# Kernel tuning notes

Measured on AMD Instinct MI355X. Metric: run time of the kernel, lower is better.

The kernel has to match this reference:

```python
import jax, jax.numpy as jnp
import numpy as np

B, S, E, H = 2, 2048, 2048, 16
NOPE, ROPE, VD = 128, 64, 128
QH = NOPE + ROPE  # 192
LORA = 512
ROPE_THETA = 10000.0
EPS = 1e-6


def setup_inputs() -> dict:
    key = jax.random.key(0)
    ks = jax.random.split(key, 5)
    sd = lambda n: 1.0 / np.sqrt(n)
    return {
        "x": jax.random.normal(ks[0], (B, S, E), jnp.float32),
        "wq": jax.random.normal(ks[1], (E, H * QH), jnp.float32) * sd(E),
        "wkv_a": jax.random.normal(ks[2], (E, LORA + ROPE), jnp.float32) * sd(E),
        "wkv_b": jax.random.normal(ks[3], (LORA, H * (NOPE + VD)), jnp.float32) * sd(LORA),
        "wo": jax.random.normal(ks[4], (H * VD, E), jnp.float32) * sd(H * VD),
        "kv_norm_scale": jnp.ones((LORA,), jnp.float32),
    }


def _rope(xp, cos, sin):
    # xp: (..., s, d); cos/sin: (s, d//2)
    d2 = xp.shape[-1] // 2
    x1, x2 = xp[..., :d2], xp[..., d2:]
    return jnp.concatenate([x1 * cos - x2 * sin, x2 * cos + x1 * sin], axis=-1)


def reference(x, wq, wkv_a, wkv_b, wo, kv_norm_scale):
    b, s, _ = x.shape
    # queries: (b, H, s, QH), split into no-pe / pe slices
    q = (x @ wq).reshape(b, s, H, QH).transpose(0, 2, 1, 3)
    q_nope, q_pe = q[..., :NOPE], q[..., NOPE:]

    # low-rank KV latent projection
    kva = x @ wkv_a  # (b, s, LORA + ROPE)
    ckv, k_pe = kva[..., :LORA], kva[..., LORA:]
    ckv = ckv * jax.lax.rsqrt(jnp.mean(ckv * ckv, axis=-1, keepdims=True) + EPS)
    ckv = ckv * kv_norm_scale  # RMSNorm on latent
    kv = (ckv @ wkv_b).reshape(b, s, H, NOPE + VD).transpose(0, 2, 1, 3)
    k_nope, v = kv[..., :NOPE], kv[..., NOPE:]

    # partial RoPE on the rope slice only
    pos = jnp.arange(s, dtype=jnp.float32)
    inv = 1.0 / (ROPE_THETA ** (jnp.arange(0, ROPE, 2, dtype=jnp.float32) / ROPE))
    ang = pos[:, None] * inv  # (s, ROPE//2)
    cos, sin = jnp.cos(ang), jnp.sin(ang)
    q_pe = _rope(q_pe, cos, sin)                 # (b, H, s, ROPE)
    k_pe = _rope(k_pe[:, None, :, :], cos, sin)  # (b, 1, s, ROPE), shared over heads

    # concat (the new_empty + slice-write in torch)
    qs = jnp.concatenate([q_nope, q_pe], axis=-1)  # (b, H, s, QH)
    ks_ = jnp.concatenate(
        [k_nope, jnp.broadcast_to(k_pe, (b, H, s, ROPE))], axis=-1
    )  # (b, H, s, QH)

    # causal SDPA with scale = q_head_dim**-0.5; asymmetric V head dim
    scale = QH ** -0.5
    scores = jnp.einsum('bhqd,bhkd->bhqk', qs, ks_) * scale
    causal = jnp.tril(jnp.ones((s, s), dtype=bool))
    scores = jnp.where(causal, scores, jnp.finfo(scores.dtype).min)
    attn = jax.nn.softmax(scores, axis=-1)
    out = jnp.einsum('bhqk,bhkd->bhqd', attn, v)  # (b, H, s, VD)
    out = out.transpose(0, 2, 1, 3).reshape(b, s, H * VD)
    return out @ wo
```

## Files before the change

### kernel.cpp

```cpp
#include <hip/hip_runtime.h>
#include <stdint.h>
#include <stddef.h>

typedef __bf16 bf16x8 __attribute__((ext_vector_type(8)));
typedef float floatx4 __attribute__((ext_vector_type(4)));
typedef unsigned short u16;

__device__ __forceinline__ float bf2f(u16 h) {
    unsigned u = ((unsigned)h) << 16;
    return __builtin_bit_cast(float, u);
}
__device__ __forceinline__ u16 f2bf(float f) {
    unsigned u = __builtin_bit_cast(unsigned, f);
    u += 0x7fffu + ((u >> 16) & 1u);
    return (u16)(u >> 16);
}

__device__ __forceinline__ void gload16(const void* g, void* l) {
    __builtin_amdgcn_global_load_lds(
        (const __attribute__((address_space(1))) uint32_t*)g,
        (__attribute__((address_space(3))) uint32_t*)l, 16, 0, 0);
}

__device__ __forceinline__ void wait_vm8() { asm volatile("s_waitcnt vmcnt(8)" ::: "memory"); }
__device__ __forceinline__ void wait_vm6() { asm volatile("s_waitcnt vmcnt(6)" ::: "memory"); }
__device__ __forceinline__ void wait_vm4() { asm volatile("s_waitcnt vmcnt(4)" ::: "memory"); }
__device__ __forceinline__ void wait_vm3() { asm volatile("s_waitcnt vmcnt(3)" ::: "memory"); }
__device__ __forceinline__ void wait_vm0() { asm volatile("s_waitcnt vmcnt(0)" ::: "memory"); }

__global__ __launch_bounds__(256) void k_conv_x(const float* __restrict__ in,
                                                u16* __restrict__ out, int n8) {
    int i = blockIdx.x * 256 + threadIdx.x;
    if (i >= n8) return;
    const float* f = in + (size_t)i * 8;
    unsigned o[4];
    for (int t = 0; t < 4; t++) {
        u16 lo = f2bf(f[2 * t]), hi = f2bf(f[2 * t + 1]);
        o[t] = (unsigned)lo | ((unsigned)hi << 16);
    }
    uint4 p = {o[0], o[1], o[2], o[3]};
    *(uint4*)&out[(size_t)i * 8] = p;
}

__global__ __launch_bounds__(256) void k_convT(const float* __restrict__ in,
                                               u16* __restrict__ out, int K, int N) {
    __shared__ u16 t[32][33];
    int k0 = blockIdx.x * 32, n0 = blockIdx.y * 32;
    int c = threadIdx.x & 31, r8 = threadIdx.x >> 5;
    for (int j = 0; j < 4; j++) {
        int row = r8 + j * 8;
        int n = n0 + c;
        t[row][c] = (n < N) ? f2bf(in[(size_t)(k0 + row) * N + n]) : (u16)0;
    }
    __syncthreads();
    for (int j = 0; j < 4; j++) {
        int row = r8 + j * 8;
        out[(size_t)(n0 + row) * K + k0 + c] = t[c][row];
    }
}

template <int NWC, int MODE>
__global__ __launch_bounds__(512, 2) void k_gemm256(const u16* __restrict__ A,
                                                    const u16* __restrict__ BT,
                                                    void* __restrict__ C0,
                                                    void* __restrict__ C1,
                                                    int K, int ldc) {
    constexpr int MFR = 16 / (8 / NWC);
    constexpr int ACH = 2;
    constexpr int BCH = NWC / 2;
    constexpr int SLOT = 8192 + NWC * 2048;
    __shared__ __align__(16) u16 RING[4][SLOT];
    int tid = threadIdx.x;
    int w = tid >> 6, lane = tid & 63;
    int l15 = lane & 15, quad = lane >> 4;
    int wr = w / NWC, wc = w % NWC;

    int gx = gridDim.x;
    int nwg = gx * gridDim.y;
    int flat = blockIdx.y * gx + blockIdx.x;
    int cpx = nwg >> 3;
    int swz = (flat & 7) * cpx + (flat >> 3);
    int bx = swz % gx, by = swz / gx;
    size_t m0 = (size_t)bx * 256, n0 = (size_t)by * (NWC * 64);
    int NT = K >> 5;

    const u16* srcA[ACH];
    const u16* srcB[BCH];
    int ldsAb[ACH], ldsBb[BCH];
#pragma unroll
    for (int p = 0; p < ACH; p++) {
        int chunk = p * 512 + tid;
        int s = chunk >> 6;
        int b = (chunk & 63) * 8;
        int bu = b ^ (((b >> 8) & 1) << 4);
        int r = bu >> 5, c = bu & 31;
        srcA[p] = A + (m0 + s * 16 + r) * (size_t)K + c;
        ldsAb[p] = (p * 512 + w * 64) * 8;
    }
#pragma unroll
    for (int p = 0; p < BCH; p++) {
        int chunk = p * 512 + tid;
        int s = chunk >> 6;
        int b = (chunk & 63) * 8;
        int bu = b ^ (((b >> 8) & 1) << 4);
        int r = bu >> 5, c = bu & 31;
        srcB[p] = BT + (n0 + s * 16 + r) * (size_t)K + c;
        ldsBb[p] = 8192 + (p * 512 + w * 64) * 8;
    }

    const int swb = (l15 * 32 + quad * 8) ^ ((l15 >> 3) << 4);

    floatx4 acc[MFR][4];
    const floatx4 fzero = {0.f, 0.f, 0.f, 0.f};
#pragma unroll
    for (int i = 0; i < MFR; i++)
#pragma unroll
        for (int j = 0; j < 4; j++) acc[i][j] = fzero;

    bf16x8 aA0[MFR], bB0[4], aA1[MFR], bB1[4];

    auto STAGE = [&](int j) {
        int rs = j & 3;
        size_t ko = (size_t)j * 32;
        u16* ring = &RING[rs][0];
#pragma unroll
        for (int p = 0; p < ACH; p++) gload16(srcA[p] + ko, ring + ldsAb[p]);
#pragma unroll
        for (int p = 0; p < BCH; p++) gload16(srcB[p] + ko, ring + ldsBb[p]);
    };
    auto READ0 = [&](int rs) {
        const u16* ring = &RING[rs][0];
#pragma unroll
        for (int i2 = 0; i2 < MFR; i2++)
            aA0[i2] = *(const bf16x8*)&ring[(wr * MFR + i2) * 512 + swb];
#pragma unroll
        for (int j2 = 0; j2 < 4; j2++)
            bB0[j2] = *(const bf16x8*)&ring[8192 + (wc * 4 + j2) * 512 + swb];
    };
    auto READ1 = [&](int rs) {
        const u16* ring = &RING[rs][0];
#pragma unroll
        for (int i2 = 0; i2 < MFR; i2++)
            aA1[i2] = *(const bf16x8*)&ring[(wr * MFR + i2) * 512 + swb];
#pragma unroll
        for (int j2 = 0; j2 < 4; j2++)
            bB1[j2] = *(const bf16x8*)&ring[8192 + (wc * 4 + j2) * 512 + swb];
    };
    auto MMA0 = [&]() {
#pragma unroll
        for (int i2 = 0; i2 < MFR; i2++)
#pragma unroll
            for (int j2 = 0; j2 < 4; j2++)
                acc[i2][j2] = __builtin_amdgcn_mfma_f32_16x16x32_bf16(
                    aA0[i2], bB0[j2], acc[i2][j2], 0, 0, 0);
    };
    auto MMA1 = [&]() {
#pragma unroll
        for (int i2 = 0; i2 < MFR; i2++)
#pragma unroll
            for (int j2 = 0; j2 < 4; j2++)
                acc[i2][j2] = __builtin_amdgcn_mfma_f32_16x16x32_bf16(
                    aA1[i2], bB1[j2], acc[i2][j2], 0, 0, 0);
    };

    STAGE(0); STAGE(1); STAGE(2);

    if constexpr (NWC == 4) {
        auto QSTEP = [&](int rs, bool doStage, int sj) {
            const u16* ring = &RING[rs][0];
#pragma unroll
            for (int i2 = 0; i2 < 4; i2++)
                aA0[i2] = *(const bf16x8*)&ring[(wr * 8 + i2) * 512 + swb];
#pragma unroll
            for (int j2 = 0; j2 < 2; j2++)
                bB0[j2] = *(const bf16x8*)&ring[8192 + (wc * 4 + j2) * 512 + swb];
            __builtin_amdgcn_sched_barrier(0);
#pragma unroll
            for (int j2 = 2; j2 < 4; j2++)
                bB0[j2] = *(const bf16x8*)&ring[8192 + (wc * 4 + j2) * 512 + swb];
            __builtin_amdgcn_sched_barrier(0);
#pragma unroll
            for (int i2 = 0; i2 < 4; i2++)
#pragma unroll
                for (int j2 = 0; j2 < 2; j2++)
                    acc[i2][j2] = __builtin_amdgcn_mfma_f32_16x16x32_bf16(
                        aA0[i2], bB0[j2], acc[i2][j2], 0, 0, 0);
            __builtin_amdgcn_sched_barrier(0);
#pragma unroll
            for (int i2 = 4; i2 < 8; i2++)
                aA0[i2] = *(const bf16x8*)&ring[(wr * 8 + i2) * 512 + swb];
            __builtin_amdgcn_sched_barrier(0);
#pragma unroll
            for (int i2 = 0; i2 < 4; i2++)
#pragma unroll
                for (int j2 = 2; j2 < 4; j2++)
                    acc[i2][j2] = __builtin_amdgcn_mfma_f32_16x16x32_bf16(
                        aA0[i2], bB0[j2], acc[i2][j2], 0, 0, 0);
            __builtin_amdgcn_sched_barrier(0);
            if (doStage) STAGE(sj);
            __builtin_amdgcn_sched_barrier(0);
#pragma unroll
            for (int i2 = 4; i2 < 8; i2++)
#pragma unroll
                for (int j2 = 2; j2 < 4; j2++)
                    acc[i2][j2] = __builtin_amdgcn_mfma_f32_16x16x32_bf16(
                        aA0[i2], bB0[j2], acc[i2][j2], 0, 0, 0);
#pragma unroll
            for (int i2 = 4; i2 < 8; i2++)
#pragma unroll
                for (int j2 = 0; j2 < 2; j2++)
                    acc[i2][j2] = __builtin_amdgcn_mfma_f32_16x16x32_bf16(
                        aA0[i2], bB0[j2], acc[i2][j2], 0, 0, 0);
        };
        int j = 0;
        for (; j + 3 < NT; j++) {
            wait_vm8();
            __builtin_amdgcn_s_barrier();
            __builtin_amdgcn_sched_barrier(0);
            QSTEP(j & 3, true, j + 3);
        }
        {
            wait_vm8();
            __builtin_amdgcn_s_barrier();
            __builtin_amdgcn_sched_barrier(0);
            QSTEP(j & 3, false, 0); j++;
        }
        {
            wait_vm4();
            __builtin_amdgcn_s_barrier();
            __builtin_amdgcn_sched_barrier(0);
            QSTEP(j & 3, false, 0); j++;
        }
        {
            wait_vm0();
            __builtin_amdgcn_s_barrier();
            __builtin_amdgcn_sched_barrier(0);
            QSTEP(j & 3, false, 0);
        }
    } else {
        wait_vm6();
        __builtin_amdgcn_s_barrier();
        __builtin_amdgcn_sched_barrier(0);
        READ0(0);
        for (int j = 0; j + 1 < NT; j += 2) {
            if (j + 2 < NT) wait_vm3(); else wait_vm0();
            __builtin_amdgcn_s_barrier();
            __builtin_amdgcn_sched_barrier(0);
            READ1((j + 1) & 3);
            if (j + 3 < NT) STAGE(j + 3);
            MMA0();
            if (j + 2 < NT) {
                if (j + 3 < NT) wait_vm3(); else wait_vm0();
                __builtin_amdgcn_s_barrier();
                __builtin_amdgcn_sched_barrier(0);
                READ0((j + 2) & 3);
                if (j + 4 < NT) STAGE(j + 4);
            }
            MMA1();
        }
    }

#pragma unroll
    for (int i = 0; i < MFR; i++)
#pragma unroll
        for (int j2 = 0; j2 < 4; j2++) {
            size_t col = n0 + wc * 64 + j2 * 16 + l15;
#pragma unroll
            for (int r = 0; r < 4; r++) {
                size_t row = m0 + (size_t)wr * (MFR * 16) + i * 16 + quad * 4 + r;
                if constexpr (MODE == 0) {
                    ((u16*)C0)[row * ldc + col] = f2bf(acc[i][j2][r]);
                } else if constexpr (MODE == 1) {
                    ((float*)C0)[row * ldc + col] = acc[i][j2][r];
                } else if constexpr (MODE == 2) {
                    if (col < 3072)
                        ((u16*)C0)[row * 3072 + col] = f2bf(acc[i][j2][r]);
                    else if (col < 3648)
                        ((u16*)C1)[row * 576 + (col - 3072)] = f2bf(acc[i][j2][r]);
                }
            }
            if constexpr (MODE == 3) {
                int cm = (int)(col & 255);
                size_t row0 = m0 + (size_t)wr * (MFR * 16) + i * 16 + quad * 4;
                if (cm < 128) {
#pragma unroll
                    for (int r = 0; r < 4; r++)
                        ((u16*)C0)[(row0 + r) * 4096 + col] = f2bf(acc[i][j2][r]);
                } else {
                    int h = (int)(col >> 8), vd = cm - 128;
                    size_t b = row0 >> 11, s = row0 & 2047;
                    unsigned lo = (unsigned)f2bf(acc[i][j2][0]) | ((unsigned)f2bf(acc[i][j2][1]) << 16);
                    unsigned hi = (unsigned)f2bf(acc[i][j2][2]) | ((unsigned)f2bf(acc[i][j2][3]) << 16);
                    uint2 pk = {lo, hi};
                    *(uint2*)&((u16*)C1)[(((b << 4) + h) * 128 + vd) * 2048 + s] = pk;
                }
            }
        }
}

__global__ __launch_bounds__(64) void k_rmsnorm(const u16* __restrict__ kva,
                                                const float* __restrict__ scl,
                                                u16* __restrict__ ckv) {
    int r = blockIdx.x, lane = threadIdx.x;
    const u16* row = kva + (size_t)r * 576 + lane * 8;
    uint4 raw = *(const uint4*)row;
    unsigned w[4] = {raw.x, raw.y, raw.z, raw.w};
    float f[8];
    float ss = 0.f;
    for (int t = 0; t < 4; t++) {
        f[2 * t]     = bf2f((u16)(w[t] & 0xffffu));
        f[2 * t + 1] = bf2f((u16)(w[t] >> 16));
        ss += f[2 * t] * f[2 * t] + f[2 * t + 1] * f[2 * t + 1];
    }
    for (int off = 1; off < 64; off <<= 1) ss += __shfl_xor(ss, off, 64);
    float rs = rsqrtf(ss * (1.f / 512.f) + 1e-6f);
    unsigned o[4];
    for (int t = 0; t < 4; t++) {
        u16 lo = f2bf(f[2 * t] * rs * scl[lane * 8 + 2 * t]);
        u16 hi = f2bf(f[2 * t + 1] * rs * scl[lane * 8 + 2 * t + 1]);
        o[t] = (unsigned)lo | ((unsigned)hi << 16);
    }
    uint4 packed = {o[0], o[1], o[2], o[3]};
    *(uint4*)(ckv + (size_t)r * 512 + lane * 8) = packed;
}

__global__ __launch_bounds__(256) void k_rope(u16* __restrict__ qbuf, u16* __restrict__ kva) {
    int tid = threadIdx.x;
    int rloc = tid >> 7;
    int task = tid & 127;
    int r = blockIdx.x * 2 + rloc;
    __shared__ float cs_s[2][32], sn_s[2][32];
    if (tid < 64) {
        int rr = tid >> 5, i = tid & 31;
        int ss = (blockIdx.x * 2 + rr) & 2047;
        float freq = __expf(-0.28782313662425575f * (float)i);
        float ang = (float)ss * freq;
        float sn, cs;
        sincosf(ang, &sn, &cs);
        cs_s[rr][i] = cs; sn_s[rr][i] = sn;
    }
    __syncthreads();
    if (task < 68) {
        int rb = task >> 2, q = task & 3;
        u16* base = (rb < 16) ? qbuf + (size_t)r * 3072 + rb * 192 + 128
                              : kva + (size_t)r * 576 + 512;
        u16* p1 = base + q * 8;
        uint4 x1v = *(uint4*)p1;
        uint4 x2v = *(uint4*)(p1 + 32);
        unsigned w1[4] = {x1v.x, x1v.y, x1v.z, x1v.w};
        unsigned w2[4] = {x2v.x, x2v.y, x2v.z, x2v.w};
        unsigned o1[4], o2[4];
        for (int t2 = 0; t2 < 4; t2++) {
            float a1 = bf2f((u16)(w1[t2] & 0xffffu)), b1 = bf2f((u16)(w1[t2] >> 16));
            float a2 = bf2f((u16)(w2[t2] & 0xffffu)), b2 = bf2f((u16)(w2[t2] >> 16));
            int i0 = q * 8 + t2 * 2, i1 = i0 + 1;
            float c0 = cs_s[rloc][i0], s0 = sn_s[rloc][i0];
            float c1 = cs_s[rloc][i1], s1 = sn_s[rloc][i1];
            o1[t2] = (unsigned)f2bf(a1 * c0 - a2 * s0) | ((unsigned)f2bf(b1 * c1 - b2 * s1) << 16);
            o2[t2] = (unsigned)f2bf(a2 * c0 + a1 * s0) | ((unsigned)f2bf(b2 * c1 + b1 * s1) << 16);
        }
        uint4 y1 = {o1[0], o1[1], o1[2], o1[3]};
        uint4 y2 = {o2[0], o2[1], o2[2], o2[3]};
        *(uint4*)p1 = y1;
        *(uint4*)(p1 + 32) = y2;
    }
}

__global__ __launch_bounds__(512, 2) void k_attn(const u16* __restrict__ qbuf,
                                                 const u16* __restrict__ kv,
                                                 const u16* __restrict__ kva,
                                                 const u16* __restrict__ vt,
                                                 u16* __restrict__ attno) {
    int tid = threadIdx.x;
    int wave = tid >> 6, lane = tid & 63;
    int quad = lane >> 4, l15 = lane & 15;
    int hb = blockIdx.x;
    int h = hb & 15, b = hb >> 4;
    int qb2 = 15 - (int)blockIdx.y;
    int qg0 = qb2 * 128 + wave * 16;
    int row = qg0 + l15;

    __shared__ __align__(16) u16 Kn[2][32 * 136];
    __shared__ __align__(16) u16 Kp[2][32 * 72];
    __shared__ __align__(16) u16 Vs[2][128 * 40];
    __shared__ __align__(16) u16 P[8][16 * 40];

    const u16* qrp = qbuf + ((size_t)(b * 2048) + qg0 + l15) * 3072 + h * 192;
    bf16x8 qf[6];
    for (int c = 0; c < 6; c++) qf[c] = *(const bf16x8*)&qrp[c * 32 + quad * 8];

    const floatx4 fzero = {0.f, 0.f, 0.f, 0.f};
    floatx4 o[8];
    for (int f = 0; f < 8; f++) o[f] = fzero;
    float lp = 0.f;
    bf16x8 vfp[8];

    const u16* kvb = kv  + (size_t)(b * 2048) * 4096 + h * 256;
    const u16* kpb = kva + (size_t)(b * 2048) * 576 + 512;
    const u16* vtb = vt  + (size_t)(b * 16 + h) * 128 * 2048;
    const float scale = 0.07216878364870323f;

    int nkt = qb2 * 4 + 4;

    int kKey = tid >> 4,  kOff = (tid & 15) * 8;
    int pKey = tid >> 3,  pOff = (tid & 7) * 8;
    bool pAct = tid < 256;
    int vRow = tid >> 2,  vOff = (tid & 3) * 8;

    {
        uint4 a = *(const uint4*)&kvb[(size_t)kKey * 4096 + kOff];
        uint4 e = *(const uint4*)&vtb[(size_t)vRow * 2048 + vOff];
        *(uint4*)&Kn[0][kKey * 136 + kOff] = a;
        *(uint4*)&Vs[0][vRow * 40 + vOff] = e;
        if (pAct) {
            uint4 d = *(const uint4*)&kpb[(size_t)pKey * 576 + pOff];
            *(uint4*)&Kp[0][pKey * 72 + pOff] = d;
        }
    }
    __syncthreads();

    for (int kt = 0; kt < nkt; kt++) {
        int cur = kt & 1;
        bool have = (kt + 1) < nkt;
        uint4 sA = {}, sC = {}, sD = {};
        if (have) {
            int kb = (kt + 1) * 32;
            sA = *(const uint4*)&kvb[(size_t)(kb + kKey) * 4096 + kOff];
            sD = *(const uint4*)&vtb[(size_t)vRow * 2048 + kb + vOff];
            if (pAct) sC = *(const uint4*)&kpb[(size_t)(kb + pKey) * 576 + pOff];
        }
        if (kt > 0 && (kt - 1) * 32 <= qg0 + 15) {
            bf16x8 pa = *(const bf16x8*)&P[wave][l15 * 40 + quad * 8];
            for (int f = 0; f < 8; f++)
                o[f] = __builtin_amdgcn_mfma_f32_16x16x32_bf16(pa, vfp[f], o[f], 0, 0, 0);
        }
        if (kt * 32 <= qg0 + 15) {
            for (int f = 0; f < 8; f++)
                vfp[f] = *(const bf16x8*)&Vs[cur][(f * 16 + l15) * 40 + quad * 8];
            floatx4 sc[2] = {fzero, fzero};
            for (int hf = 0; hf < 2; hf++) {
                const u16* kn = &Kn[cur][(hf * 16 + l15) * 136];
                const u16* kp = &Kp[cur][(hf * 16 + l15) * 72];
                for (int c = 0; c < 4; c++) {
                    bf16x8 kf = *(const bf16x8*)&kn[c * 32 + quad * 8];
                    sc[hf] = __builtin_amdgcn_mfma_f32_16x16x32_bf16(kf, qf[c], sc[hf], 0, 0, 0);
                }
                for (int c = 0; c < 2; c++) {
                    bf16x8 kf = *(const bf16x8*)&kp[c * 32 + quad * 8];
                    sc[hf] = __builtin_amdgcn_mfma_f32_16x16x32_bf16(kf, qf[4 + c], sc[hf], 0, 0, 0);
                }
            }
            asm volatile("" ::: "memory");
            for (int hf = 0; hf < 2; hf++) {
                int keyb = kt * 32 + hf * 16 + quad * 4;
                float p[4];
                for (int r = 0; r < 4; r++)
                    p[r] = (keyb + r <= row) ? __expf(sc[hf][r] * scale) : 0.f;
                lp += (p[0] + p[1]) + (p[2] + p[3]);
                unsigned d0 = (unsigned)f2bf(p[0]) | ((unsigned)f2bf(p[1]) << 16);
                unsigned d1 = (unsigned)f2bf(p[2]) | ((unsigned)f2bf(p[3]) << 16);
                uint2 pk = {d0, d1};
                *(uint2*)&P[wave][l15 * 40 + hf * 16 + quad * 4] = pk;
            }
            asm volatile("" ::: "memory");
        }
        if (have) {
            int nb = cur ^ 1;
            *(uint4*)&Kn[nb][kKey * 136 + kOff] = sA;
            *(uint4*)&Vs[nb][vRow * 40 + vOff] = sD;
            if (pAct) *(uint4*)&Kp[nb][pKey * 72 + pOff] = sC;
        }
        __syncthreads();
    }
    if ((nkt - 1) * 32 <= qg0 + 15) {
        bf16x8 pa = *(const bf16x8*)&P[wave][l15 * 40 + quad * 8];
        for (int f = 0; f < 8; f++)
            o[f] = __builtin_amdgcn_mfma_f32_16x16x32_bf16(pa, vfp[f], o[f], 0, 0, 0);
    }

    lp += __shfl_xor(lp, 16, 64);
    lp += __shfl_xor(lp, 32, 64);
    float lrow[4];
    for (int r = 0; r < 4; r++) lrow[r] = __shfl(lp, quad * 4 + r, 64);
    for (int f = 0; f < 8; f++)
        for (int r = 0; r < 4; r++) {
            int orow = qg0 + quad * 4 + r;
            float val = o[f][r] / lrow[r];
            attno[((size_t)(b * 2048) + orow) * 2048 + h * 128 + f * 16 + l15] = f2bf(val);
        }
}

extern "C" void kernel_launch(void* const* d_in, const int* in_sizes, int n_in,
                              void* d_out, int out_size, void* d_ws, size_t ws_size,
                              hipStream_t stream) {
    const float* x_raw    = (const float*)d_in[0];
    const float* wq_raw   = (const float*)d_in[1];
    const float* wkva_raw = (const float*)d_in[2];
    const float* wkvb_raw = (const float*)d_in[3];
    const float* wo_raw   = (const float*)d_in[4];
    const float* kvs_raw  = (const float*)d_in[5];
    float* out = (float*)d_out;
    u16* ws = (u16*)d_ws;

    const size_t O_ATT = 0;
    const size_t O_VT  = 8388608;
    const size_t O_QB  = 16777216;
    const size_t O_KVA = 29360128;
    const size_t O_KV  = 31719424;
    const size_t TOTAL_BYTES = 48496640ull * 2;
    if (ws_size < TOTAL_BYTES) return;

    u16* g12bt  = ws + O_ATT;
    u16* ckv    = ws + O_ATT;
    u16* wkvb_t = ws + O_ATT + 2097152;
    u16* attno  = ws + O_ATT;
    u16* x_bf   = ws + O_VT;
    u16* vt     = ws + O_VT;
    u16* qbuf   = ws + O_QB;
    u16* wo_t   = ws + O_QB;
    u16* kva    = ws + O_KVA;
    u16* kv     = ws + O_KV;

    k_conv_x<<<4096, 256, 0, stream>>>(x_raw, x_bf, 1048576);
    k_convT<<<dim3(64, 96), 256, 0, stream>>>(wq_raw, g12bt, 2048, 3072);
    k_convT<<<dim3(64, 24), 256, 0, stream>>>(wkva_raw, g12bt + (size_t)3072 * 2048, 2048, 576);

    k_gemm256<4, 2><<<dim3(16, 15), 512, 0, stream>>>(x_bf, g12bt, qbuf, kva, 2048, 0);

    k_rmsnorm<<<4096, 64, 0, stream>>>(kva, kvs_raw, ckv);
    k_convT<<<dim3(16, 128), 256, 0, stream>>>(wkvb_raw, wkvb_t, 512, 4096);
    k_gemm256<4, 3><<<dim3(16, 16), 512, 0, stream>>>(ckv, wkvb_t, kv, vt, 512, 4096);

    k_rope<<<2048, 256, 0, stream>>>(qbuf, kva);

    k_attn<<<dim3(32, 16), 512, 0, stream>>>(qbuf, kv, kva, vt, attno);

    k_convT<<<dim3(64, 64), 256, 0, stream>>>(wo_raw, wo_t, 2048, 2048);
    k_gemm256<2, 1><<<dim3(16, 16), 512, 0, stream>>>(attno, wo_t, out, nullptr, 2048, 2048);
}
```

Before: 369.5 us.

## Shrink attention blocks to 64 query rows with 256 threads

```diff
diff --git a/kernel.cpp b/kernel.cpp
--- a/kernel.cpp
+++ b/kernel.cpp
@@ -366,7 +366,7 @@
     }
 }
 
-__global__ __launch_bounds__(512, 2) void k_attn(const u16* __restrict__ qbuf,
+__global__ __launch_bounds__(256, 3) void k_attn(const u16* __restrict__ qbuf,
                                                  const u16* __restrict__ kv,
                                                  const u16* __restrict__ kva,
                                                  const u16* __restrict__ vt,
@@ -376,14 +376,14 @@
     int quad = lane >> 4, l15 = lane & 15;
     int hb = blockIdx.x;
     int h = hb & 15, b = hb >> 4;
-    int qb2 = 15 - (int)blockIdx.y;
-    int qg0 = qb2 * 128 + wave * 16;
+    int qb = 31 - (int)blockIdx.y;
+    int qg0 = qb * 64 + wave * 16;
     int row = qg0 + l15;
 
     __shared__ __align__(16) u16 Kn[2][32 * 136];
     __shared__ __align__(16) u16 Kp[2][32 * 72];
     __shared__ __align__(16) u16 Vs[2][128 * 40];
-    __shared__ __align__(16) u16 P[8][16 * 40];
+    __shared__ __align__(16) u16 P[4][16 * 40];
 
     const u16* qrp = qbuf + ((size_t)(b * 2048) + qg0 + l15) * 3072 + h * 192;
     bf16x8 qf[6];
@@ -400,34 +400,39 @@
     const u16* vtb = vt  + (size_t)(b * 16 + h) * 128 * 2048;
     const float scale = 0.07216878364870323f;
 
-    int nkt = qb2 * 4 + 4;
-
-    int kKey = tid >> 4,  kOff = (tid & 15) * 8;
-    int pKey = tid >> 3,  pOff = (tid & 7) * 8;
-    bool pAct = tid < 256;
-    int vRow = tid >> 2,  vOff = (tid & 3) * 8;
+    int nkt = qb * 2 + 2;
+
+    int kKey0 = tid >> 4,          kOff0 = (tid & 15) * 8;
+    int kKey1 = (tid + 256) >> 4,  kOff1 = (tid & 15) * 8;
+    int pKey  = tid >> 3,          pOff  = (tid & 7) * 8;
+    int vRow0 = tid >> 2,          vOff0 = (tid & 3) * 8;
+    int vRow1 = (tid + 256) >> 2,  vOff1 = (tid & 3) * 8;
 
     {
-        uint4 a = *(const uint4*)&kvb[(size_t)kKey * 4096 + kOff];
-        uint4 e = *(const uint4*)&vtb[(size_t)vRow * 2048 + vOff];
-        *(uint4*)&Kn[0][kKey * 136 + kOff] = a;
-        *(uint4*)&Vs[0][vRow * 40 + vOff] = e;
-        if (pAct) {
-            uint4 d = *(const uint4*)&kpb[(size_t)pKey * 576 + pOff];
-            *(uint4*)&Kp[0][pKey * 72 + pOff] = d;
-        }
+        uint4 a = *(const uint4*)&kvb[(size_t)kKey0 * 4096 + kOff0];
+        uint4 c = *(const uint4*)&kvb[(size_t)kKey1 * 4096 + kOff1];
+        uint4 d = *(const uint4*)&kpb[(size_t)pKey * 576 + pOff];
+        uint4 e = *(const uint4*)&vtb[(size_t)vRow0 * 2048 + vOff0];
+        uint4 g = *(const uint4*)&vtb[(size_t)vRow1 * 2048 + vOff1];
+        *(uint4*)&Kn[0][kKey0 * 136 + kOff0] = a;
+        *(uint4*)&Kn[0][kKey1 * 136 + kOff1] = c;
+        *(uint4*)&Kp[0][pKey * 72 + pOff] = d;
+        *(uint4*)&Vs[0][vRow0 * 40 + vOff0] = e;
+        *(uint4*)&Vs[0][vRow1 * 40 + vOff1] = g;
     }
     __syncthreads();
 
     for (int kt = 0; kt < nkt; kt++) {
         int cur = kt & 1;
         bool have = (kt + 1) < nkt;
-        uint4 sA = {}, sC = {}, sD = {};
+        uint4 sA = {}, sB = {}, sC = {}, sD = {}, sE = {};
         if (have) {
             int kb = (kt + 1) * 32;
-            sA = *(const uint4*)&kvb[(size_t)(kb + kKey) * 4096 + kOff];
-            sD = *(const uint4*)&vtb[(size_t)vRow * 2048 + kb + vOff];
-            if (pAct) sC = *(const uint4*)&kpb[(size_t)(kb + pKey) * 576 + pOff];
+            sA = *(const uint4*)&kvb[(size_t)(kb + kKey0) * 4096 + kOff0];
+            sB = *(const uint4*)&kvb[(size_t)(kb + kKey1) * 4096 + kOff1];
+            sC = *(const uint4*)&kpb[(size_t)(kb + pKey) * 576 + pOff];
+            sD = *(const uint4*)&vtb[(size_t)vRow0 * 2048 + kb + vOff0];
+            sE = *(const uint4*)&vtb[(size_t)vRow1 * 2048 + kb + vOff1];
         }
         if (kt > 0 && (kt - 1) * 32 <= qg0 + 15) {
             bf16x8 pa = *(const bf16x8*)&P[wave][l15 * 40 + quad * 8];
@@ -466,9 +471,11 @@
         }
         if (have) {
             int nb = cur ^ 1;
-            *(uint4*)&Kn[nb][kKey * 136 + kOff] = sA;
-            *(uint4*)&Vs[nb][vRow * 40 + vOff] = sD;
-            if (pAct) *(uint4*)&Kp[nb][pKey * 72 + pOff] = sC;
+            *(uint4*)&Kn[nb][kKey0 * 136 + kOff0] = sA;
+            *(uint4*)&Kn[nb][kKey1 * 136 + kOff1] = sB;
+            *(uint4*)&Kp[nb][pKey * 72 + pOff] = sC;
+            *(uint4*)&Vs[nb][vRow0 * 40 + vOff0] = sD;
+            *(uint4*)&Vs[nb][vRow1 * 40 + vOff1] = sE;
         }
         __syncthreads();
     }
@@ -533,7 +540,7 @@
 
     k_rope<<<2048, 256, 0, stream>>>(qbuf, kva);
 
-    k_attn<<<dim3(32, 16), 512, 0, stream>>>(qbuf, kv, kva, vt, attno);
+    k_attn<<<dim3(32, 32), 256, 0, stream>>>(qbuf, kv, kva, vt, attno);
 
     k_convT<<<dim3(64, 64), 256, 0, stream>>>(wo_raw, wo_t, 2048, 2048);
     k_gemm256<2, 1><<<dim3(16, 16), 512, 0, stream>>>(attno, wo_t, out, nullptr, 2048, 2048);
```

New measurement: 355.2 us. -3.9%, faster.
